# Performance work log

Hardware: AMD Instinct MI355X
Metric: run time of the kernel (lower is better)

The kernel has to match this reference:

```python
import jax, jax.numpy as jnp
import numpy as np

NUM_HEADS = 8
LN_EPS = 1e-5


def _ln(x, g, b):
    mu = x.mean(-1, keepdims=True)
    xc = x - mu
    v = (xc * xc).mean(-1, keepdims=True)
    return xc * jax.lax.rsqrt(v + LN_EPS) * g + b


def setup_inputs() -> dict:
    key = jax.random.key(0)
    B, T, D, NI, NT = 16, 512, 256, 85, 77
    L, FF, TH = 2, 1024, 32
    ks = iter(jax.random.split(key, 40))
    def nrm(shape, std):
        return jax.random.normal(next(ks), shape, jnp.float32) * std
    inp = {
        'img_tokens': nrm((B, NI, D), 1.0),
        'text_tokens': nrm((B, NT, D), 1.0),
        'task_tokens': nrm((T, D), 0.02),
        'type_task': nrm((D,), 0.02),
        'type_img': nrm((D,), 0.02),
        'type_txt': nrm((D,), 0.02),
        'in_ln_g': jnp.ones((D,), jnp.float32), 'in_ln_b': jnp.zeros((D,), jnp.float32),
        'Wqkv': nrm((L, 3 * D, D), 1.0 / np.sqrt(D)), 'bqkv': jnp.zeros((L, 3 * D), jnp.float32),
        'Wo': nrm((L, D, D), 1.0 / np.sqrt(D)), 'bo': jnp.zeros((L, D), jnp.float32),
        'ln1_g': jnp.ones((L, D), jnp.float32), 'ln1_b': jnp.zeros((L, D), jnp.float32),
        'ln2_g': jnp.ones((L, D), jnp.float32), 'ln2_b': jnp.zeros((L, D), jnp.float32),
        'W1': nrm((L, FF, D), 1.0 / np.sqrt(D)), 'b1': jnp.zeros((L, FF), jnp.float32),
        'W2': nrm((L, D, FF), 1.0 / np.sqrt(FF)), 'b2': jnp.zeros((L, D), jnp.float32),
        'out_ln_g': jnp.ones((D,), jnp.float32), 'out_ln_b': jnp.zeros((D,), jnp.float32),
        'tw1': nrm((T, TH, D), 1.0 / np.sqrt(D)), 'tb1': jnp.zeros((T, TH), jnp.float32),
        'tw2': nrm((T, TH), 1.0 / np.sqrt(TH)), 'tb2': jnp.zeros((T,), jnp.float32),
        'text_mask': jnp.arange(NT)[None, :] < jax.random.randint(next(ks), (B, 1), 10, NT + 1),
        'labels': jax.random.randint(next(ks), (B, T), -1, 2),
    }
    return inp


def reference(img_tokens, text_tokens, task_tokens, type_task, type_img, type_txt,
              in_ln_g, in_ln_b, Wqkv, bqkv, Wo, bo, ln1_g, ln1_b, ln2_g, ln2_b,
              W1, b1, W2, b2, out_ln_g, out_ln_b, tw1, tb1, tw2, tb2,
              text_mask, labels):
    B, NI, D = img_tokens.shape
    T = task_tokens.shape[0]
    L = Wqkv.shape[0]
    hd = D // NUM_HEADS
    available = labels != -1                                   # (B, T)
    n_avail = available.sum(axis=1)                            # (B,)
    # Route B: stable-sort available task ids to the front (permutation per row)
    order = jnp.argsort((~available).astype(jnp.int32), axis=1, stable=True)  # (B, T)
    task_toks = task_tokens[order] + type_task                 # (B, T, D)
    seq = jnp.concatenate([task_toks, img_tokens + type_img, text_tokens + type_txt], axis=1)
    seq = _ln(seq, in_ln_g, in_ln_b)
    task_pad = jnp.arange(T)[None, :] >= n_avail[:, None]
    pad = jnp.concatenate([task_pad, jnp.zeros((B, NI), bool), ~text_mask], axis=1)
    bias = jnp.where(pad, -1e9, 0.0).astype(seq.dtype)[:, None, None, :]  # key-padding mask
    scale = 1.0 / np.sqrt(hd)
    S = seq.shape[1]
    for l in range(L):  # pre-LN transformer encoder layers (eval mode)
        h = _ln(seq, ln1_g[l], ln1_b[l])
        qkv = h @ Wqkv[l].T + bqkv[l]
        q, k, v = jnp.split(qkv, 3, axis=-1)
        q = q.reshape(B, S, NUM_HEADS, hd)
        k = k.reshape(B, S, NUM_HEADS, hd)
        v = v.reshape(B, S, NUM_HEADS, hd)
        scores = jnp.einsum('bqhd,bkhd->bhqk', q, k) * scale + bias
        attn = jax.nn.softmax(scores, axis=-1)
        o = jnp.einsum('bhqk,bkhd->bqhd', attn, v).reshape(B, S, D)
        seq = seq + o @ Wo[l].T + bo[l]
        h2 = _ln(seq, ln2_g[l], ln2_b[l])
        seq = seq + jax.nn.gelu(h2 @ W1[l].T + b1[l], approximate=False) @ W2[l].T + b2[l]
    task_out = _ln(seq[:, :T], out_ln_g, out_ln_b)             # (B, T, D)
    # undo the per-row permutation so task t's token sits at column t, then
    # apply all per-task towers as one grouped matmul (MoE dispatch/combine)
    y = jnp.zeros_like(task_out).at[jnp.arange(B)[:, None], order].set(task_out)
    hsz = jax.nn.relu(jnp.einsum('btd,thd->bth', y, tw1) + tb1[None])
    out = jnp.einsum('bth,th->bt', hsz, tw2) + tb2[None]
    return jnp.where(available, out, jnp.zeros((), out.dtype))
```

## Files before the change

kernel.cpp:

```cpp
#include <hip/hip_runtime.h>
#include <hip/hip_bf16.h>
#include <math.h>

constexpr int B_  = 16;
constexpr int T_  = 512;
constexpr int D_  = 256;
constexpr int NI_ = 85;
constexpr int NT_ = 77;
constexpr int S_  = T_ + NI_ + NT_;
constexpr int M_  = B_ * S_;
constexpr int FF_ = 1024;
constexpr int TH_ = 32;
constexpr int NH_ = 8;
constexpr int KT_ = 704;
constexpr int NKT_ = KT_ / 64;

constexpr float MASK_NEG = -30000.0f;

constexpr int N_FT = 26;
constexpr int OFF_[N_FT + 1] = {
    0,
    348160,
    663552,
    794624,
    794880,
    795136,
    795392,
    795648,
    795904,
    1189120,
    1190656,
    1321728,
    1322240,
    1322752,
    1323264,
    1323776,
    1324288,
    1848576,
    1850624,
    2374912,
    2375424,
    2375680,
    2375936,
    6570240,
    6586624,
    6603008,
    6603520
};
constexpr int TOTAL_ELEMS = OFF_[N_FT];

typedef __attribute__((ext_vector_type(8))) short bfrag;
typedef __attribute__((ext_vector_type(4))) float f32x4;

__device__ inline float bf2f(__hip_bfloat16 x) { return __bfloat162float(x); }
__device__ inline __hip_bfloat16 f2bf(float x) { return __float2bfloat16(x); }
__device__ inline float wsum64(float v) {
    #pragma unroll
    for (int m = 32; m >= 1; m >>= 1) v += __shfl_xor(v, m, 64);
    return v;
}
__device__ inline bool is_f32_mode(const void* ln_g_raw) {
    return (*(const unsigned int*)ln_g_raw) == 0x3F800000u;
}

__device__ inline void gload_lds16(const __hip_bfloat16* g, __hip_bfloat16* l) {
#if defined(__has_builtin) && __has_builtin(__builtin_amdgcn_global_load_lds)
    __builtin_amdgcn_global_load_lds(
        (const __attribute__((address_space(1))) unsigned int*)g,
        (__attribute__((address_space(3))) unsigned int*)l, 16, 0, 0);
#else
    *reinterpret_cast<uint4*>(l) = *reinterpret_cast<const uint4*>(g);
#endif
}

struct Ptrs { const void* p[N_FT]; };

__global__ __launch_bounds__(256) void k_convert(Ptrs ptrs, __hip_bfloat16* __restrict__ canon) {
    int idx = blockIdx.x * 256 + threadIdx.x;
    if (idx >= TOTAL_ELEMS) return;
    bool f32 = is_f32_mode(ptrs.p[6]);
    int t = 0;
    #pragma unroll
    for (int i = 1; i < N_FT; i++) if (idx >= OFF_[i]) t = i;
    int local = idx - OFF_[t];
    if (f32) canon[idx] = f2bf(((const float*)ptrs.p[t])[local]);
    else     canon[idx] = ((const __hip_bfloat16*)ptrs.p[t])[local];
}

__global__ void k_prep(const int* __restrict__ labels, int* __restrict__ inv,
                       int* __restrict__ n_avail) {
    __shared__ int sc[T_];
    int b = blockIdx.x, t = threadIdx.x;
    int av = (labels[b * T_ + t] != -1) ? 1 : 0;
    sc[t] = av;
    __syncthreads();
    for (int off = 1; off < T_; off <<= 1) {
        int v = sc[t];
        int u = (t >= off) ? sc[t - off] : 0;
        __syncthreads();
        sc[t] = v + u;
        __syncthreads();
    }
    int incl  = sc[t];
    int excl  = incl - av;
    int total = sc[T_ - 1];
    inv[b * T_ + t] = av ? excl : (total + (t - excl));
    if (t == 0) n_avail[b] = total;
}

__global__ void k_build(const __hip_bfloat16* __restrict__ img,
                        const __hip_bfloat16* __restrict__ txt,
                        const __hip_bfloat16* __restrict__ task,
                        const __hip_bfloat16* __restrict__ ty_task,
                        const __hip_bfloat16* __restrict__ ty_img,
                        const __hip_bfloat16* __restrict__ ty_txt,
                        const __hip_bfloat16* __restrict__ g,
                        const __hip_bfloat16* __restrict__ bln,
                        const __hip_bfloat16* __restrict__ g1,
                        const __hip_bfloat16* __restrict__ b1,
                        const void* __restrict__ text_mask,
                        const int* __restrict__ inv,
                        const int* __restrict__ n_avail,
                        float* __restrict__ seq,
                        __hip_bfloat16* __restrict__ h1,
                        float* __restrict__ bias) {
    int blk = blockIdx.x;
    int b = blk / S_, j = blk % S_;
    int lane = threadIdx.x;

    int dest;
    float bias_v;
    const __hip_bfloat16* src;
    const __hip_bfloat16* tvec;
    if (j < T_) {
        dest = inv[b * T_ + j];
        src = task + (size_t)j * D_;
        tvec = ty_task;
        bias_v = (dest >= n_avail[b]) ? MASK_NEG : 0.f;
    } else if (j < T_ + NI_) {
        dest = j;
        src = img + (size_t)(b * NI_ + (j - T_)) * D_;
        tvec = ty_img;
        bias_v = 0.f;
    } else {
        int x2 = j - T_ - NI_;
        dest = j;
        src = txt + (size_t)(b * NT_ + x2) * D_;
        tvec = ty_txt;
        const unsigned char* mb = (const unsigned char*)text_mask;
        bool is_byte = (mb[1] != 0);
        int mv = is_byte ? (int)mb[b * NT_ + x2]
                         : ((const int*)text_mask)[b * NT_ + x2];
        bias_v = mv ? 0.f : MASK_NEG;
    }

    float x[4];
    float s = 0.f, ss = 0.f;
    #pragma unroll
    for (int i = 0; i < 4; i++) {
        int d = lane * 4 + i;
// ... 32 lines not shown
    *reinterpret_cast<uint2*>(h1 + ((size_t)b * S_ + dest) * D_ + lane * 4) =
        *reinterpret_cast<uint2*>(tmp);
    if (lane == 0) bias[b * S_ + dest] = bias_v;
}

template <int GELU>
__global__ __launch_bounds__(256) void k_gemm(const __hip_bfloat16* __restrict__ A,
                                              const __hip_bfloat16* __restrict__ W,
                                              const __hip_bfloat16* __restrict__ bias,
                                              __hip_bfloat16* __restrict__ Cout,
                                              int Mm, int N, int K) {
    __shared__ __align__(16) unsigned char Sh[24576];
    __hip_bfloat16* As = (__hip_bfloat16*)Sh;
    __hip_bfloat16* Ws = (__hip_bfloat16*)(Sh + 8192);
    __hip_bfloat16* Es = (__hip_bfloat16*)Sh;

    int m0 = blockIdx.x * 64;
    int n0 = blockIdx.y * 128;
    int tid = threadIdx.x;
    int w = tid >> 6, lane = tid & 63;
    int lrow = lane & 15, quad = lane >> 4;

    f32x4 acc[8] = {};

    int kq = (tid & 7) * 8;
    int arow = tid >> 3;
    const __hip_bfloat16* Ar0 = A + (size_t)min(m0 + arow,      Mm - 1) * K + kq;
    const __hip_bfloat16* Ar1 = A + (size_t)min(m0 + arow + 32, Mm - 1) * K + kq;
    __hip_bfloat16* Al0 = As + tid * 8;
    __hip_bfloat16* Al1 = As + (tid + 256) * 8;
    const __hip_bfloat16* Wr[4];
    __hip_bfloat16* Wl[4];
    #pragma unroll
    for (int i = 0; i < 4; i++) {
        int c = tid + i * 256;
        Wr[i] = W + (size_t)(n0 + (c >> 3)) * K + kq;
        Wl[i] = Ws + c * 8;
    }

    for (int k0 = 0; k0 < K; k0 += 64) {
        __syncthreads();
        gload_lds16(Ar0 + k0, Al0);
        gload_lds16(Ar1 + k0, Al1);
        #pragma unroll
        for (int i = 0; i < 4; i++) gload_lds16(Wr[i] + k0, Wl[i]);
        __syncthreads();

        #pragma unroll
        for (int ko = 0; ko < 2; ko++) {
            bfrag af = *reinterpret_cast<const bfrag*>(&As[(w * 16 + lrow) * 64 + ko * 32 + quad * 8]);
            #pragma unroll
            for (int nt = 0; nt < 8; nt++) {
                bfrag bf = *reinterpret_cast<const bfrag*>(&Ws[(nt * 16 + lrow) * 64 + ko * 32 + quad * 8]);
                acc[nt] = __builtin_amdgcn_mfma_f32_16x16x32_bf16(af, bf, acc[nt], 0, 0, 0);
            }
        }
    }
    __syncthreads();

    #pragma unroll
    for (int nt = 0; nt < 8; nt++) {
        int col = nt * 16 + lrow;
        float bv = bf2f(bias[n0 + col]);
        #pragma unroll
        for (int rg = 0; rg < 4; rg++) {
            int row = w * 16 + quad * 4 + rg;
            float v = acc[nt][rg] + bv;
            if (GELU) v = 0.5f * v * (1.f + erff(v * 0.70710678118654752f));
            Es[row * 136 + col] = f2bf(v);
        }
    }
    __syncthreads();

    #pragma unroll
    for (int i = 0; i < 4; i++) {
        int c = tid + i * 256;
        int row = c >> 4, off = (c & 15) * 8;
        int gm = m0 + row;
        if (gm < Mm) {
            uint4 v4 = *reinterpret_cast<const uint4*>(&Es[row * 136 + off]);
            *reinterpret_cast<uint4*>(&Cout[(size_t)gm * N + n0 + off]) = v4;
        }
    }
}

template <int LNOUT>
__global__ __launch_bounds__(256) void k_gemm_lnres(const __hip_bfloat16* __restrict__ A,
                                                    const __hip_bfloat16* __restrict__ W,
                                                    const __hip_bfloat16* __restrict__ bias,
                                                    float* __restrict__ seq,
                                                    const __hip_bfloat16* __restrict__ lng,
                                                    const __hip_bfloat16* __restrict__ lnb,
                                                    __hip_bfloat16* __restrict__ lnout,
                                                    int K) {
    constexpr int N = 256;
    constexpr int ESTRIDE = 260;
    __shared__ __align__(16) unsigned char Sh[36864];
    __hip_bfloat16* As = (__hip_bfloat16*)Sh;
    __hip_bfloat16* Ws = (__hip_bfloat16*)(Sh + 4096);
    float*          Es = (float*)Sh;

    int m0 = blockIdx.x * 32;
    int tid = threadIdx.x;
    int w = tid >> 6, lane = tid & 63;
    int lrow = lane & 15, quad = lane >> 4;

    f32x4 acc[2][4] = {};

    int kq = (tid & 7) * 8;
    const __hip_bfloat16* Ar = A + (size_t)(m0 + (tid >> 3)) * K + kq;
    __hip_bfloat16* Al = As + tid * 8;
    const __hip_bfloat16* Wr[8];
    __hip_bfloat16* Wl[8];
    #pragma unroll
    for (int i = 0; i < 8; i++) {
        int c = tid + i * 256;
        Wr[i] = W + (size_t)(c >> 3) * K + kq;
        Wl[i] = Ws + c * 8;
    }

    for (int k0 = 0; k0 < K; k0 += 64) {
        __syncthreads();
        gload_lds16(Ar + k0, Al);
        #pragma unroll
        for (int i = 0; i < 8; i++) gload_lds16(Wr[i] + k0, Wl[i]);
        __syncthreads();

        #pragma unroll
        for (int ko = 0; ko < 2; ko++) {
            bfrag af[2], bf[4];
            #pragma unroll
            for (int mt = 0; mt < 2; mt++)
                af[mt] = *reinterpret_cast<const bfrag*>(&As[(mt * 16 + lrow) * 64 + ko * 32 + quad * 8]);
            #pragma unroll
            for (int nt = 0; nt < 4; nt++)
                bf[nt] = *reinterpret_cast<const bfrag*>(&Ws[(w * 64 + nt * 16 + lrow) * 64 + ko * 32 + quad * 8]);
            #pragma unroll
            for (int mt = 0; mt < 2; mt++)
                #pragma unroll
                for (int nt = 0; nt < 4; nt++)
                    acc[mt][nt] = __builtin_amdgcn_mfma_f32_16x16x32_bf16(af[mt], bf[nt], acc[mt][nt], 0, 0, 0);
        }
    }
    __syncthreads();

    #pragma unroll
    for (int nt = 0; nt < 4; nt++) {
        int col = w * 64 + nt * 16 + lrow;
        float bv = bf2f(bias[col]);
        #pragma unroll
        for (int mt = 0; mt < 2; mt++)
            #pragma unroll
            for (int rg = 0; rg < 4; rg++)
                Es[(mt * 16 + quad * 4 + rg) * ESTRIDE + col] = acc[mt][nt][rg] + bv;
    }
    __syncthreads();

    int row = tid >> 3, part = tid & 7;
    size_t gm = (size_t)(m0 + row);
    float* seqrow = seq + gm * N + part * 32;
    float t[32];
    float s = 0.f, ss = 0.f;
    #pragma unroll
    for (int j = 0; j < 8; j++) {
        float4 e = *reinterpret_cast<const float4*>(&Es[row * ESTRIDE + part * 32 + j * 4]);
        float4 r4 = *reinterpret_cast<const float4*>(&seqrow[j * 4]);
        float v0 = e.x + r4.x, v1 = e.y + r4.y, v2 = e.z + r4.z, v3 = e.w + r4.w;
        t[j * 4 + 0] = v0; t[j * 4 + 1] = v1; t[j * 4 + 2] = v2; t[j * 4 + 3] = v3;
        s += v0 + v1 + v2 + v3;
        ss += v0 * v0 + v1 * v1 + v2 * v2 + v3 * v3;
    }
    #pragma unroll
    for (int j = 0; j < 8; j++) {
        float4 o = make_float4(t[j * 4 + 0], t[j * 4 + 1], t[j * 4 + 2], t[j * 4 + 3]);
        *reinterpret_cast<float4*>(&seqrow[j * 4]) = o;
    }
    if (LNOUT) {
        #pragma unroll
        for (int mm = 4; mm >= 1; mm >>= 1) {
            s  += __shfl_xor(s,  mm, 8);
            ss += __shfl_xor(ss, mm, 8);
        }
        float mean = s * (1.f / N);
        float var  = ss * (1.f / N) - mean * mean;
        float r    = rsqrtf(fmaxf(var, 0.f) + 1e-5f);
        __hip_bfloat16 ob[32];
        #pragma unroll
        for (int j = 0; j < 32; j++) {
            int col = part * 32 + j;
            ob[j] = f2bf((t[j] - mean) * r * bf2f(lng[col]) + bf2f(lnb[col]));
        }
        #pragma unroll
        for (int j = 0; j < 4; j++)
            *reinterpret_cast<uint4*>(&lnout[gm * N + part * 32 + j * 8]) =
                *reinterpret_cast<const uint4*>(&ob[j * 8]);
    }
}

__global__ __launch_bounds__(256) void k_fattn(const __hip_bfloat16* __restrict__ qkv,
                                               const float* __restrict__ bias,
                                               __hip_bfloat16* __restrict__ out) {
    __shared__ __align__(16) __hip_bfloat16 Vt[2][32 * 72];
    __shared__ __align__(16) __hip_bfloat16 Ps[4][16 * 72];
    __shared__ float Bs[KT_];
    __shared__ int alive[NKT_];
    __shared__ int tlist[NKT_ + 1];
    __shared__ int nact_s;
    int b = blockIdx.z, h = blockIdx.y;
    int tid = threadIdx.x;
    int wave = tid >> 6, lane = tid & 63;
    int lrow = lane & 15, quad = lane >> 4;
    int q0 = blockIdx.x * 64 + wave * 16;

    const float scale = 0.17677669529663687f;
    const __hip_bfloat16* base = qkv + (size_t)b * S_ * 768;
    const float* brow = bias + b * S_;

    for (int i = tid; i < KT_; i += 256) Bs[i] = (i < S_) ? brow[i] : MASK_NEG;
    if (tid < NKT_) alive[tid] = 0;
    __syncthreads();
    for (int i = tid; i < KT_; i += 256)
        if (Bs[i] != MASK_NEG) alive[i >> 6] = 1;
    __syncthreads();
    if (tid == 0) {
        int n = 0;
        for (int t = 0; t < NKT_; t++) if (alive[t]) tlist[n++] = t;
        if (n == 0) { tlist[0] = 0; n = 1; }
        tlist[n] = tlist[n - 1];
        nact_s = n;
    }
    __syncthreads();
    int nact = nact_s;

    int qr = q0 + lrow; if (qr >= S_) qr = S_ - 1;
    bfrag qf = *reinterpret_cast<const bfrag*>(base + (size_t)qr * 768 + h * 32 + quad * 8);

    bfrag ones_f;
    #pragma unroll
    for (int i = 0; i < 8; i++) ((short*)&ones_f)[i] = (short)0x3F80;

    float m[4] = {-3e38f, -3e38f, -3e38f, -3e38f};
    f32x4 Lacc = {};
    f32x4 O[2] = {};

    int skey = lane;
    int sd   = wave * 8;

    bfrag kf_cur[4], vv_cur;
    {
        int k0 = tlist[0] * 64;
        #pragma unroll
        for (int nt = 0; nt < 4; nt++) {
            int kr = min(k0 + nt * 16 + lrow, S_ - 1);
            kf_cur[nt] = *reinterpret_cast<const bfrag*>(base + (size_t)kr * 768 + 256 + h * 32 + quad * 8);
        }
        int kr = min(k0 + skey, S_ - 1);
        vv_cur = *reinterpret_cast<const bfrag*>(base + (size_t)kr * 768 + 512 + h * 32 + sd);
    }

    for (int i = 0; i < nact; i++) {
        int k0 = tlist[i] * 64;
        __hip_bfloat16* vb = Vt[i & 1];

        #pragma unroll
        for (int j = 0; j < 8; j++) vb[(sd + j) * 72 + skey] = ((const __hip_bfloat16*)&vv_cur)[j];
        __syncthreads();

        bfrag kf_nxt[4], vv_nxt;
        {
            int kb = tlist[i + 1] * 64;
            #pragma unroll
            for (int nt = 0; nt < 4; nt++) {
                int kr = min(kb + nt * 16 + lrow, S_ - 1);
                kf_nxt[nt] = *reinterpret_cast<const bfrag*>(base + (size_t)kr * 768 + 256 + h * 32 + quad * 8);
            }
            int kr = min(kb + skey, S_ - 1);
            vv_nxt = *reinterpret_cast<const bfrag*>(base + (size_t)kr * 768 + 512 + h * 32 + sd);
        }

        f32x4 sc4[4];
        #pragma unroll
        for (int nt = 0; nt < 4; nt++) {
            f32x4 z = {};
            sc4[nt] = __builtin_amdgcn_mfma_f32_16x16x32_bf16(qf, kf_cur[nt], z, 0, 0, 0);
            float bv = Bs[k0 + nt * 16 + lrow];
            #pragma unroll
            for (int rg = 0; rg < 4; rg++) sc4[nt][rg] = sc4[nt][rg] * scale + bv;
        }

        float alpha[4];
        #pragma unroll
        for (int rg = 0; rg < 4; rg++) {
            float rm = fmaxf(fmaxf(sc4[0][rg], sc4[1][rg]), fmaxf(sc4[2][rg], sc4[3][rg]));
            #pragma unroll
            for (int mm2 = 1; mm2 <= 8; mm2 <<= 1) rm = fmaxf(rm, __shfl_xor(rm, mm2, 64));
            float mn = fmaxf(m[rg], rm);
            alpha[rg] = __expf(m[rg] - mn);
            m[rg] = mn;
            #pragma unroll
            for (int nt = 0; nt < 4; nt++) sc4[nt][rg] = __expf(sc4[nt][rg] - mn);
        }
        #pragma unroll
        for (int rg = 0; rg < 4; rg++) {
            O[0][rg] *= alpha[rg];
            O[1][rg] *= alpha[rg];
            Lacc[rg] *= alpha[rg];
        }

        #pragma unroll
        for (int nt = 0; nt < 4; nt++)
            #pragma unroll
            for (int rg = 0; rg < 4; rg++)
                Ps[wave][(quad * 4 + rg) * 72 + nt * 16 + lrow] = f2bf(sc4[nt][rg]);

        bfrag ap0 = *reinterpret_cast<const bfrag*>(&Ps[wave][lrow * 72 + quad * 8]);
        bfrag ap1 = *reinterpret_cast<const bfrag*>(&Ps[wave][lrow * 72 + 32 + quad * 8]);
        #pragma unroll
        for (int dt = 0; dt < 2; dt++) {
            bfrag bv0 = *reinterpret_cast<const bfrag*>(&vb[(dt * 16 + lrow) * 72 + quad * 8]);
            bfrag bv1 = *reinterpret_cast<const bfrag*>(&vb[(dt * 16 + lrow) * 72 + 32 + quad * 8]);
            O[dt] = __builtin_amdgcn_mfma_f32_16x16x32_bf16(ap0, bv0, O[dt], 0, 0, 0);
            O[dt] = __builtin_amdgcn_mfma_f32_16x16x32_bf16(ap1, bv1, O[dt], 0, 0, 0);
        }
        Lacc = __builtin_amdgcn_mfma_f32_16x16x32_bf16(ap0, ones_f, Lacc, 0, 0, 0);
        Lacc = __builtin_amdgcn_mfma_f32_16x16x32_bf16(ap1, ones_f, Lacc, 0, 0, 0);

        #pragma unroll
        for (int nt = 0; nt < 4; nt++) kf_cur[nt] = kf_nxt[nt];
        vv_cur = vv_nxt;
    }

    #pragma unroll
    for (int rg = 0; rg < 4; rg++) {
        int qrow = q0 + quad * 4 + rg;
        if (qrow < S_) {
            float invl = 1.f / Lacc[rg];
            #pragma unroll
            for (int dt = 0; dt < 2; dt++)
                out[((size_t)b * S_ + qrow) * D_ + h * 32 + dt * 16 + lrow] = f2bf(O[dt][rg] * invl);
        }
    }
}

__global__ __launch_bounds__(256) void k_final(const float* __restrict__ seq,
                                               const int* __restrict__ inv,
                                               const int* __restrict__ labels,
                                               const __hip_bfloat16* __restrict__ g,
                                               const __hip_bfloat16* __restrict__ bb,
                                               const __hip_bfloat16* __restrict__ tw1,
                                               const __hip_bfloat16* __restrict__ tb1,
                                               const __hip_bfloat16* __restrict__ tw2,
                                               const __hip_bfloat16* __restrict__ tb2,
                                               const void* __restrict__ ln_g_raw,
                                               void* __restrict__ out) {
    int idx = blockIdx.x;
    int t = idx >> 4, b = idx & 15;
    int tid = threadIdx.x;
    bool f32o = is_f32_mode(ln_g_raw);

    int lab = labels[b * T_ + t];
    if (lab == -1) {
        if (tid == 0) {
            if (f32o) ((float*)out)[b * T_ + t] = 0.f;
            else      ((__hip_bfloat16*)out)[b * T_ + t] = f2bf(0.f);
        }
        return;
    }

    __shared__ float y[D_];
    __shared__ float hb[TH_];
    __shared__ float rs[4], rq[4];

    int row = inv[b * T_ + t];
    float x = seq[((size_t)b * S_ + row) * D_ + tid];
    float s1 = wsum64(x);
    float s2 = wsum64(x * x);
    int w = tid >> 6, lane = tid & 63;
    if (lane == 0) { rs[w] = s1; rq[w] = s2; }
    __syncthreads();
    float fs = rs[0] + rs[1] + rs[2] + rs[3];
    float fq = rq[0] + rq[1] + rq[2] + rq[3];
    float mean = fs * (1.f / D_);
    float var  = fq * (1.f / D_) - mean * mean;
    float r    = rsqrtf(fmaxf(var, 0.f) + 1e-5f);
    y[tid] = (x - mean) * r * bf2f(g[tid]) + bf2f(bb[tid]);
    __syncthreads();

    int hh = tid >> 3, part = tid & 7;
    const uint4* w4 = reinterpret_cast<const uint4*>(tw1 + ((size_t)t * TH_ + hh) * D_ + part * 32);
    float acc = 0.f;
    #pragma unroll
    for (int i = 0; i < 4; i++) {
        uint4 kv = w4[i];
        unsigned int wd[4] = {kv.x, kv.y, kv.z, kv.w};
        #pragma unroll
        for (int j2 = 0; j2 < 4; j2++) {
            unsigned int lo = wd[j2] << 16, hi = wd[j2] & 0xffff0000u;
            float flo, fhi;
            __builtin_memcpy(&flo, &lo, 4);
            __builtin_memcpy(&fhi, &hi, 4);
            acc += y[part * 32 + i * 8 + j2 * 2] * flo;
            acc += y[part * 32 + i * 8 + j2 * 2 + 1] * fhi;
        }
    }
    #pragma unroll
    for (int mm = 4; mm >= 1; mm >>= 1) acc += __shfl_down(acc, mm, 8);
    if (part == 0) {
        float hz = acc + bf2f(tb1[t * TH_ + hh]);
        hz = fmaxf(hz, 0.f);
        hb[hh] = hz * bf2f(tw2[t * TH_ + hh]);
    }
    __syncthreads();
    if (tid == 0) {
        float o = bf2f(tb2[t]);
        #pragma unroll
        for (int i = 0; i < TH_; i++) o += hb[i];
        if (f32o) ((float*)out)[b * T_ + t] = o;
        else      ((__hip_bfloat16*)out)[b * T_ + t] = f2bf(o);
    }
}

extern "C" void kernel_launch(void* const* d_in, const int* in_sizes, int n_in,
                              void* d_out, int out_size, void* d_ws, size_t ws_size,
                              hipStream_t stream) {
    const void* tmask  = d_in[26];
    const int*  labels = (const int*)d_in[27];

    char* p = (char*)d_ws;
    auto alloc = [&](size_t bytes) {
        char* r = p;
        p += (bytes + 255) & ~size_t(255);
        return r;
    };
    __hip_bfloat16* canon  = (__hip_bfloat16*)alloc(sizeof(__hip_bfloat16) * (size_t)TOTAL_ELEMS);
    int*            inv     = (int*)alloc(sizeof(int) * B_ * T_);
    int*            n_avail = (int*)alloc(sizeof(int) * B_);
    float*          bias    = (float*)alloc(sizeof(float) * M_);
    float*          seqF    = (float*)alloc(sizeof(float) * (size_t)M_ * D_);
    __hip_bfloat16* bufA    = (__hip_bfloat16*)alloc(sizeof(__hip_bfloat16) * (size_t)M_ * D_);
    __hip_bfloat16* bufBig  = (__hip_bfloat16*)alloc(sizeof(__hip_bfloat16) * (size_t)M_ * FF_);

    Ptrs ptrs;
    for (int i = 0; i < N_FT; i++) ptrs.p[i] = d_in[i];
    hipLaunchKernelGGL(k_convert, dim3((TOTAL_ELEMS + 255) / 256), dim3(256), 0, stream,
                       ptrs, canon);

    const __hip_bfloat16* img      = canon + OFF_[0];
    const __hip_bfloat16* txt      = canon + OFF_[1];
    const __hip_bfloat16* task     = canon + OFF_[2];
    const __hip_bfloat16* ty_task  = canon + OFF_[3];
    const __hip_bfloat16* ty_img   = canon + OFF_[4];
    const __hip_bfloat16* ty_txt   = canon + OFF_[5];
    const __hip_bfloat16* in_ln_g  = canon + OFF_[6];
    const __hip_bfloat16* in_ln_b  = canon + OFF_[7];
    const __hip_bfloat16* Wqkv     = canon + OFF_[8];
    const __hip_bfloat16* bqkv     = canon + OFF_[9];
    const __hip_bfloat16* Wo       = canon + OFF_[10];
    const __hip_bfloat16* bo       = canon + OFF_[11];
    const __hip_bfloat16* ln1_g    = canon + OFF_[12];
    const __hip_bfloat16* ln1_b    = canon + OFF_[13];
    const __hip_bfloat16* ln2_g    = canon + OFF_[14];
    const __hip_bfloat16* ln2_b    = canon + OFF_[15];
    const __hip_bfloat16* W1       = canon + OFF_[16];
    const __hip_bfloat16* b1       = canon + OFF_[17];
    const __hip_bfloat16* W2       = canon + OFF_[18];
    const __hip_bfloat16* b2       = canon + OFF_[19];
    const __hip_bfloat16* out_ln_g = canon + OFF_[20];
    const __hip_bfloat16* out_ln_b = canon + OFF_[21];
    const __hip_bfloat16* tw1      = canon + OFF_[22];
    const __hip_bfloat16* tb1      = canon + OFF_[23];
    const __hip_bfloat16* tw2      = canon + OFF_[24];
    const __hip_bfloat16* tb2      = canon + OFF_[25];

    hipLaunchKernelGGL(k_prep, dim3(B_), dim3(T_), 0, stream, labels, inv, n_avail);
    hipLaunchKernelGGL(k_build, dim3(B_ * S_), dim3(64), 0, stream,
                       img, txt, task, ty_task, ty_img, ty_txt, in_ln_g, in_ln_b,
                       ln1_g, ln1_b, tmask, inv, n_avail, seqF, bufA, bias);

    const int mtiles = (M_ + 63) / 64;
    const int rtiles = M_ / 32;
    const int qtiles = (S_ + 63) / 64;

    for (int l = 0; l < 2; l++) {
        hipLaunchKernelGGL((k_gemm<0>), dim3(mtiles, 6), dim3(256), 0, stream,
                           bufA, Wqkv + (size_t)l * 3 * D_ * D_, bqkv + l * 3 * D_,
                           bufBig, M_, 3 * D_, D_);
        hipLaunchKernelGGL(k_fattn, dim3(qtiles, NH_, B_), dim3(256), 0, stream,
                           bufBig, bias, bufA);
        hipLaunchKernelGGL((k_gemm_lnres<1>), dim3(rtiles), dim3(256), 0, stream,
                           bufA, Wo + (size_t)l * D_ * D_, bo + l * D_, seqF,
                           ln2_g + l * D_, ln2_b + l * D_, bufA, D_);
        hipLaunchKernelGGL((k_gemm<1>), dim3(mtiles, 8), dim3(256), 0, stream,
                           bufA, W1 + (size_t)l * FF_ * D_, b1 + l * FF_,
                           bufBig, M_, FF_, D_);
        if (l == 0) {
            hipLaunchKernelGGL((k_gemm_lnres<1>), dim3(rtiles), dim3(256), 0, stream,
                               bufBig, W2 + (size_t)l * D_ * FF_, b2 + l * D_, seqF,
                               ln1_g + 1 * D_, ln1_b + 1 * D_, bufA, FF_);
        } else {
            hipLaunchKernelGGL((k_gemm_lnres<0>), dim3(rtiles), dim3(256), 0, stream,
                               bufBig, W2 + (size_t)l * D_ * FF_, b2 + l * D_, seqF,
                               (const __hip_bfloat16*)nullptr, (const __hip_bfloat16*)nullptr,
                               (__hip_bfloat16*)nullptr, FF_);
        }
    }

    hipLaunchKernelGGL(k_final, dim3(T_ * B_), dim3(256), 0, stream,
                       seqF, inv, labels, out_ln_g, out_ln_b,
                       tw1, tb1, tw2, tb2, d_in[6], d_out);
}
```

Before: 403.4 us.

## Fuse out-projection, LN2, FFN up/GELU/down and residual into one tail kernel

Replaces the Wo GEMM+LN kernel, the W1 GELU GEMM and the W2 GEMM+residual kernel with a single per-32-row kernel. The attention tile, the LN2 output and the FFN hidden activations (in two 512-column halves) stay in shared memory. This removes the large M×1024 hidden-activation round trip through global memory and two launches. In exchange, weight fragments are read directly from global memory without LDS staging, and each 32-row block rereads the full Wo/W1/W2, so it relies on cache hits. Larger LDS use may also lower occupancy.

```diff
diff --git a/kernel.cpp b/kernel.cpp
--- a/kernel.cpp
+++ b/kernel.cpp
@@ -54,6 +54,9 @@
 
 __device__ inline float bf2f(__hip_bfloat16 x) { return __bfloat162float(x); }
 __device__ inline __hip_bfloat16 f2bf(float x) { return __float2bfloat16(x); }
+__device__ inline f32x4 mfma16(bfrag a, bfrag b, f32x4 c) {
+    return __builtin_amdgcn_mfma_f32_16x16x32_bf16(a, b, c, 0, 0, 0);
+}
 __device__ inline float wsum64(float v) {
     #pragma unroll
     for (int m = 32; m >= 1; m >>= 1) v += __shfl_xor(v, m, 64);
@@ -244,7 +247,7 @@
             #pragma unroll
             for (int nt = 0; nt < 8; nt++) {
                 bfrag bf = *reinterpret_cast<const bfrag*>(&Ws[(nt * 16 + lrow) * 64 + ko * 32 + quad * 8]);
-                acc[nt] = __builtin_amdgcn_mfma_f32_16x16x32_bf16(af, bf, acc[nt], 0, 0, 0);
+                acc[nt] = mfma16(af, bf, acc[nt]);
             }
         }
     }
@@ -277,115 +280,197 @@
 }
 
 template <int LNOUT>
-__global__ __launch_bounds__(256) void k_gemm_lnres(const __hip_bfloat16* __restrict__ A,
-                                                    const __hip_bfloat16* __restrict__ W,
-                                                    const __hip_bfloat16* __restrict__ bias,
-                                                    float* __restrict__ seq,
-                                                    const __hip_bfloat16* __restrict__ lng,
-                                                    const __hip_bfloat16* __restrict__ lnb,
-                                                    __hip_bfloat16* __restrict__ lnout,
-                                                    int K) {
-    constexpr int N = 256;
-    constexpr int ESTRIDE = 260;
-    __shared__ __align__(16) unsigned char Sh[36864];
-    __hip_bfloat16* As = (__hip_bfloat16*)Sh;
-    __hip_bfloat16* Ws = (__hip_bfloat16*)(Sh + 4096);
-    float*          Es = (float*)Sh;
+__global__ __launch_bounds__(256) void k_tail(const __hip_bfloat16* __restrict__ attn,
+                                              const __hip_bfloat16* __restrict__ Wo,
+                                              const __hip_bfloat16* __restrict__ bo,
+                                              float* __restrict__ seq,
+                                              const __hip_bfloat16* __restrict__ ln2g,
+                                              const __hip_bfloat16* __restrict__ ln2b,
+                                              const __hip_bfloat16* __restrict__ W1,
+                                              const __hip_bfloat16* __restrict__ b1,
+                                              const __hip_bfloat16* __restrict__ W2,
+                                              const __hip_bfloat16* __restrict__ b2,
+                                              const __hip_bfloat16* __restrict__ lng,
+                                              const __hip_bfloat16* __restrict__ lnb,
+                                              __hip_bfloat16* __restrict__ hout) {
+    constexpr int ASTR = 264;
+    constexpr int FSTR = 520;
+    constexpr int ESTR = 260;
+    __shared__ __align__(16) unsigned char Sh[16896 + 33280];
+    __hip_bfloat16* Atile = (__hip_bfloat16*)Sh;
+    __hip_bfloat16* h2    = (__hip_bfloat16*)Sh;
+    __hip_bfloat16* fh    = (__hip_bfloat16*)(Sh + 16896);
+    float*          Es    = (float*)(Sh + 16896);
 
     int m0 = blockIdx.x * 32;
     int tid = threadIdx.x;
-    int w = tid >> 6, lane = tid & 63;
+    int wave = tid >> 6, lane = tid & 63;
     int lrow = lane & 15, quad = lane >> 4;
 
-    f32x4 acc[2][4] = {};
-
-    int kq = (tid & 7) * 8;
-    const __hip_bfloat16* Ar = A + (size_t)(m0 + (tid >> 3)) * K + kq;
-    __hip_bfloat16* Al = As + tid * 8;
-    const __hip_bfloat16* Wr[8];
-    __hip_bfloat16* Wl[8];
-    #pragma unroll
-    for (int i = 0; i < 8; i++) {
+    #pragma unroll
+    for (int i = 0; i < 4; i++) {
         int c = tid + i * 256;
-        Wr[i] = W + (size_t)(c >> 3) * K + kq;
-        Wl[i] = Ws + c * 8;
-    }
-
-    for (int k0 = 0; k0 < K; k0 += 64) {
-        __syncthreads();
-        gload_lds16(Ar + k0, Al);
-        #pragma unroll
-        for (int i = 0; i < 8; i++) gload_lds16(Wr[i] + k0, Wl[i]);
-        __syncthreads();
-
-        #pragma unroll
-        for (int ko = 0; ko < 2; ko++) {
-            bfrag af[2], bf[4];
-            #pragma unroll
-            for (int mt = 0; mt < 2; mt++)
-                af[mt] = *reinterpret_cast<const bfrag*>(&As[(mt * 16 + lrow) * 64 + ko * 32 + quad * 8]);
-            #pragma unroll
-            for (int nt = 0; nt < 4; nt++)
-                bf[nt] = *reinterpret_cast<const bfrag*>(&Ws[(w * 64 + nt * 16 + lrow) * 64 + ko * 32 + quad * 8]);
+        int row = c >> 5;
+        int off = (c & 31) * 8;
+        uint4 v = *reinterpret_cast<const uint4*>(attn + (size_t)(m0 + row) * 256 + off);
+        *reinterpret_cast<uint4*>(&Atile[row * ASTR + off]) = v;
+    }
+    __syncthreads();
+
+    int wn = wave * 64;
+    {
+        f32x4 a1[2][4] = {};
+        for (int k = 0; k < 8; k++) {
+            bfrag af0 = *reinterpret_cast<const bfrag*>(&Atile[lrow * ASTR + k * 32 + quad * 8]);
+            bfrag af1 = *reinterpret_cast<const bfrag*>(&Atile[(16 + lrow) * ASTR + k * 32 + quad * 8]);
+            #pragma unroll
+            for (int nt = 0; nt < 4; nt++) {
+                bfrag bf = *reinterpret_cast<const bfrag*>(Wo + (size_t)(wn + nt * 16 + lrow) * 256 + k * 32 + quad * 8);
+                a1[0][nt] = mfma16(af0, bf, a1[0][nt]);
+                a1[1][nt] = mfma16(af1, bf, a1[1][nt]);
+            }
+        }
+        #pragma unroll
+        for (int nt = 0; nt < 4; nt++) {
+            int col = wn + nt * 16 + lrow;
+            float bv = bf2f(bo[col]);
             #pragma unroll
             for (int mt = 0; mt < 2; mt++)
                 #pragma unroll
-                for (int nt = 0; nt < 4; nt++)
-                    acc[mt][nt] = __builtin_amdgcn_mfma_f32_16x16x32_bf16(af[mt], bf[nt], acc[mt][nt], 0, 0, 0);
-        }
-    }
-    __syncthreads();
-
-    #pragma unroll
-    for (int nt = 0; nt < 4; nt++) {
-        int col = w * 64 + nt * 16 + lrow;
-        float bv = bf2f(bias[col]);
-        #pragma unroll
-        for (int mt = 0; mt < 2; mt++)
-            #pragma unroll
-            for (int rg = 0; rg < 4; rg++)
-                Es[(mt * 16 + quad * 4 + rg) * ESTRIDE + col] = acc[mt][nt][rg] + bv;
-    }
-    __syncthreads();
-
-    int row = tid >> 3, part = tid & 7;
-    size_t gm = (size_t)(m0 + row);
-    float* seqrow = seq + gm * N + part * 32;
-    float t[32];
-    float s = 0.f, ss = 0.f;
-    #pragma unroll
-    for (int j = 0; j < 8; j++) {
-        float4 e = *reinterpret_cast<const float4*>(&Es[row * ESTRIDE + part * 32 + j * 4]);
-        float4 r4 = *reinterpret_cast<const float4*>(&seqrow[j * 4]);
-        float v0 = e.x + r4.x, v1 = e.y + r4.y, v2 = e.z + r4.z, v3 = e.w + r4.w;
-        t[j * 4 + 0] = v0; t[j * 4 + 1] = v1; t[j * 4 + 2] = v2; t[j * 4 + 3] = v3;
-        s += v0 + v1 + v2 + v3;
-        ss += v0 * v0 + v1 * v1 + v2 * v2 + v3 * v3;
-    }
-    #pragma unroll
-    for (int j = 0; j < 8; j++) {
-        float4 o = make_float4(t[j * 4 + 0], t[j * 4 + 1], t[j * 4 + 2], t[j * 4 + 3]);
-        *reinterpret_cast<float4*>(&seqrow[j * 4]) = o;
-    }
-    if (LNOUT) {
+                for (int rg = 0; rg < 4; rg++)
+                    Es[(mt * 16 + quad * 4 + rg) * ESTR + col] = a1[mt][nt][rg] + bv;
+        }
+    }
+    __syncthreads();
+
+    {
+        int row = tid >> 3, part = tid & 7;
+        size_t gm = (size_t)(m0 + row);
+        float* srow = seq + gm * 256 + part * 32;
+        float t[32];
+        float s = 0.f, ss = 0.f;
+        #pragma unroll
+        for (int j = 0; j < 8; j++) {
+            float4 e = *reinterpret_cast<const float4*>(&Es[row * ESTR + part * 32 + j * 4]);
+            float4 r = *reinterpret_cast<const float4*>(&srow[j * 4]);
+            float v0 = e.x + r.x, v1 = e.y + r.y, v2 = e.z + r.z, v3 = e.w + r.w;
+            t[j * 4] = v0; t[j * 4 + 1] = v1; t[j * 4 + 2] = v2; t[j * 4 + 3] = v3;
+            s += v0 + v1 + v2 + v3;
+            ss += v0 * v0 + v1 * v1 + v2 * v2 + v3 * v3;
+            *reinterpret_cast<float4*>(&srow[j * 4]) = make_float4(v0, v1, v2, v3);
+        }
         #pragma unroll
         for (int mm = 4; mm >= 1; mm >>= 1) {
             s  += __shfl_xor(s,  mm, 8);
             ss += __shfl_xor(ss, mm, 8);
         }
-        float mean = s * (1.f / N);
-        float var  = ss * (1.f / N) - mean * mean;
-        float r    = rsqrtf(fmaxf(var, 0.f) + 1e-5f);
+        float mean = s * (1.f / 256.f);
+        float var  = ss * (1.f / 256.f) - mean * mean;
+        float rr   = rsqrtf(fmaxf(var, 0.f) + 1e-5f);
         __hip_bfloat16 ob[32];
         #pragma unroll
         for (int j = 0; j < 32; j++) {
             int col = part * 32 + j;
-            ob[j] = f2bf((t[j] - mean) * r * bf2f(lng[col]) + bf2f(lnb[col]));
+            ob[j] = f2bf((t[j] - mean) * rr * bf2f(ln2g[col]) + bf2f(ln2b[col]));
         }
         #pragma unroll
         for (int j = 0; j < 4; j++)
-            *reinterpret_cast<uint4*>(&lnout[gm * N + part * 32 + j * 8]) =
+            *reinterpret_cast<uint4*>(&h2[row * ASTR + part * 32 + j * 8]) =
                 *reinterpret_cast<const uint4*>(&ob[j * 8]);
+    }
+    __syncthreads();
+
+    int wn1 = wave * 128;
+    f32x4 a4[2][4] = {};
+    for (int half = 0; half < 2; half++) {
+        f32x4 a3[2][8] = {};
+        for (int k = 0; k < 8; k++) {
+            bfrag af0 = *reinterpret_cast<const bfrag*>(&h2[lrow * ASTR + k * 32 + quad * 8]);
+            bfrag af1 = *reinterpret_cast<const bfrag*>(&h2[(16 + lrow) * ASTR + k * 32 + quad * 8]);
+            #pragma unroll
+            for (int nt = 0; nt < 8; nt++) {
+                int n = half * 512 + wn1 + nt * 16 + lrow;
+                bfrag bf = *reinterpret_cast<const bfrag*>(W1 + (size_t)n * 256 + k * 32 + quad * 8);
+                a3[0][nt] = mfma16(af0, bf, a3[0][nt]);
+                a3[1][nt] = mfma16(af1, bf, a3[1][nt]);
+            }
+        }
+        __syncthreads();
+        #pragma unroll
+        for (int nt = 0; nt < 8; nt++) {
+            int lcol = wn1 + nt * 16 + lrow;
+            float bv = bf2f(b1[half * 512 + lcol]);
+            #pragma unroll
+            for (int mt = 0; mt < 2; mt++)
+                #pragma unroll
+                for (int rg = 0; rg < 4; rg++) {
+                    float v = a3[mt][nt][rg] + bv;
+                    v = 0.5f * v * (1.f + erff(v * 0.70710678118654752f));
+                    fh[(mt * 16 + quad * 4 + rg) * FSTR + lcol] = f2bf(v);
+                }
+        }
+        __syncthreads();
+        for (int k = 0; k < 16; k++) {
+            bfrag af0 = *reinterpret_cast<const bfrag*>(&fh[lrow * FSTR + k * 32 + quad * 8]);
+            bfrag af1 = *reinterpret_cast<const bfrag*>(&fh[(16 + lrow) * FSTR + k * 32 + quad * 8]);
+            #pragma unroll
+            for (int nt = 0; nt < 4; nt++) {
+                bfrag bf = *reinterpret_cast<const bfrag*>(W2 + (size_t)(wn + nt * 16 + lrow) * 1024 + half * 512 + k * 32 + quad * 8);
+                a4[0][nt] = mfma16(af0, bf, a4[0][nt]);
+                a4[1][nt] = mfma16(af1, bf, a4[1][nt]);
+            }
+        }
+    }
+    __syncthreads();
+
+    #pragma unroll
+    for (int nt = 0; nt < 4; nt++) {
+        int col = wn + nt * 16 + lrow;
+        float bv = bf2f(b2[col]);
+        #pragma unroll
+        for (int mt = 0; mt < 2; mt++)
+            #pragma unroll
+            for (int rg = 0; rg < 4; rg++)
+                Es[(mt * 16 + quad * 4 + rg) * ESTR + col] = a4[mt][nt][rg] + bv;
+    }
+    __syncthreads();
+
+    {
+        int row = tid >> 3, part = tid & 7;
+        size_t gm = (size_t)(m0 + row);
+        float* srow = seq + gm * 256 + part * 32;
+        float t[32];
+        float s = 0.f, ss = 0.f;
+        #pragma unroll
+        for (int j = 0; j < 8; j++) {
+            float4 e = *reinterpret_cast<const float4*>(&Es[row * ESTR + part * 32 + j * 4]);
+            float4 r = *reinterpret_cast<const float4*>(&srow[j * 4]);
+            float v0 = e.x + r.x, v1 = e.y + r.y, v2 = e.z + r.z, v3 = e.w + r.w;
+            t[j * 4] = v0; t[j * 4 + 1] = v1; t[j * 4 + 2] = v2; t[j * 4 + 3] = v3;
+            s += v0 + v1 + v2 + v3;
+            ss += v0 * v0 + v1 * v1 + v2 * v2 + v3 * v3;
+            *reinterpret_cast<float4*>(&srow[j * 4]) = make_float4(v0, v1, v2, v3);
+        }
+        if (LNOUT) {
+            #pragma unroll
+            for (int mm = 4; mm >= 1; mm >>= 1) {
+                s  += __shfl_xor(s,  mm, 8);
+                ss += __shfl_xor(ss, mm, 8);
+            }
+            float mean = s * (1.f / 256.f);
+            float var  = ss * (1.f / 256.f) - mean * mean;
+            float rr   = rsqrtf(fmaxf(var, 0.f) + 1e-5f);
+            __hip_bfloat16 ob[32];
+            #pragma unroll
+            for (int j = 0; j < 32; j++) {
+                int col = part * 32 + j;
+                ob[j] = f2bf((t[j] - mean) * rr * bf2f(lng[col]) + bf2f(lnb[col]));
+            }
+            #pragma unroll
+            for (int j = 0; j < 4; j++)
+                *reinterpret_cast<uint4*>(&hout[gm * 256 + part * 32 + j * 8]) =
+                    *reinterpret_cast<const uint4*>(&ob[j * 8]);
+        }
     }
 }
 
@@ -474,7 +559,7 @@
         #pragma unroll
         for (int nt = 0; nt < 4; nt++) {
             f32x4 z = {};
-            sc4[nt] = __builtin_amdgcn_mfma_f32_16x16x32_bf16(qf, kf_cur[nt], z, 0, 0, 0);
+            sc4[nt] = mfma16(qf, kf_cur[nt], z);
             float bv = Bs[k0 + nt * 16 + lrow];
             #pragma unroll
             for (int rg = 0; rg < 4; rg++) sc4[nt][rg] = sc4[nt][rg] * scale + bv;
@@ -511,11 +596,11 @@
         for (int dt = 0; dt < 2; dt++) {
             bfrag bv0 = *reinterpret_cast<const bfrag*>(&vb[(dt * 16 + lrow) * 72 + quad * 8]);
             bfrag bv1 = *reinterpret_cast<const bfrag*>(&vb[(dt * 16 + lrow) * 72 + 32 + quad * 8]);
-            O[dt] = __builtin_amdgcn_mfma_f32_16x16x32_bf16(ap0, bv0, O[dt], 0, 0, 0);
-            O[dt] = __builtin_amdgcn_mfma_f32_16x16x32_bf16(ap1, bv1, O[dt], 0, 0, 0);
-        }
-        Lacc = __builtin_amdgcn_mfma_f32_16x16x32_bf16(ap0, ones_f, Lacc, 0, 0, 0);
-        Lacc = __builtin_amdgcn_mfma_f32_16x16x32_bf16(ap1, ones_f, Lacc, 0, 0, 0);
+            O[dt] = mfma16(ap0, bv0, O[dt]);
+            O[dt] = mfma16(ap1, bv1, O[dt]);
+        }
+        Lacc = mfma16(ap0, ones_f, Lacc);
+        Lacc = mfma16(ap1, ones_f, Lacc);
 
         #pragma unroll
         for (int nt = 0; nt < 4; nt++) kf_cur[nt] = kf_nxt[nt];
@@ -630,7 +715,7 @@
     float*          bias    = (float*)alloc(sizeof(float) * M_);
     float*          seqF    = (float*)alloc(sizeof(float) * (size_t)M_ * D_);
     __hip_bfloat16* bufA    = (__hip_bfloat16*)alloc(sizeof(__hip_bfloat16) * (size_t)M_ * D_);
-    __hip_bfloat16* bufBig  = (__hip_bfloat16*)alloc(sizeof(__hip_bfloat16) * (size_t)M_ * FF_);
+    __hip_bfloat16* bufBig  = (__hip_bfloat16*)alloc(sizeof(__hip_bfloat16) * (size_t)M_ * 3 * D_);
 
     Ptrs ptrs;
     for (int i = 0; i < N_FT; i++) ptrs.p[i] = d_in[i];
@@ -679,21 +764,21 @@
                            bufBig, M_, 3 * D_, D_);
         hipLaunchKernelGGL(k_fattn, dim3(qtiles, NH_, B_), dim3(256), 0, stream,
                            bufBig, bias, bufA);
-        hipLaunchKernelGGL((k_gemm_lnres<1>), dim3(rtiles), dim3(256), 0, stream,
-                           bufA, Wo + (size_t)l * D_ * D_, bo + l * D_, seqF,
-                           ln2_g + l * D_, ln2_b + l * D_, bufA, D_);
-        hipLaunchKernelGGL((k_gemm<1>), dim3(mtiles, 8), dim3(256), 0, stream,
-                           bufA, W1 + (size_t)l * FF_ * D_, b1 + l * FF_,
-                           bufBig, M_, FF_, D_);
         if (l == 0) {
-            hipLaunchKernelGGL((k_gemm_lnres<1>), dim3(rtiles), dim3(256), 0, stream,
-                               bufBig, W2 + (size_t)l * D_ * FF_, b2 + l * D_, seqF,
-                               ln1_g + 1 * D_, ln1_b + 1 * D_, bufA, FF_);
+            hipLaunchKernelGGL((k_tail<1>), dim3(rtiles), dim3(256), 0, stream,
+                               bufA, Wo + (size_t)l * D_ * D_, bo + l * D_, seqF,
+                               ln2_g + l * D_, ln2_b + l * D_,
+                               W1 + (size_t)l * FF_ * D_, b1 + l * FF_,
+                               W2 + (size_t)l * D_ * FF_, b2 + l * D_,
+                               ln1_g + 1 * D_, ln1_b + 1 * D_, bufA);
         } else {
-            hipLaunchKernelGGL((k_gemm_lnres<0>), dim3(rtiles), dim3(256), 0, stream,
-                               bufBig, W2 + (size_t)l * D_ * FF_, b2 + l * D_, seqF,
+            hipLaunchKernelGGL((k_tail<0>), dim3(rtiles), dim3(256), 0, stream,
+                               bufA, Wo + (size_t)l * D_ * D_, bo + l * D_, seqF,
+                               ln2_g + l * D_, ln2_b + l * D_,
+                               W1 + (size_t)l * FF_ * D_, b1 + l * FF_,
+                               W2 + (size_t)l * D_ * FF_, b2 + l * D_,
                                (const __hip_bfloat16*)nullptr, (const __hip_bfloat16*)nullptr,
-                               (__hip_bfloat16*)nullptr, FF_);
+                               (__hip_bfloat16*)nullptr);
         }
     }
 
```

Measured after the change: 505.6 us. 25.3% more time.

## Double query rows per attention wave and merge convert/prep kernels

Applied to the files above, without the earlier changes.

Each attention wave now handles 32 query rows (two 16-row MFMA tiles) instead of 16, so every K/V tile it loads and stages is reused across twice as many queries. The query tile per block grows to 128 and the grid shrinks by half. The bias load and alive-tile detection are folded into one loop. The input conversion and label prefix-scan kernels are merged into one launch to remove a launch. The trade-off is more registers and LDS per wave and fewer blocks, which may lower occupancy.

```diff
diff --git a/kernel.cpp b/kernel.cpp
--- a/kernel.cpp
+++ b/kernel.cpp
@@ -48,6 +48,7 @@
     6603520
 };
 constexpr int TOTAL_ELEMS = OFF_[N_FT];
+constexpr int CONV_BLOCKS = (TOTAL_ELEMS + 511) / 512;
 
 typedef __attribute__((ext_vector_type(8))) short bfrag;
 typedef __attribute__((ext_vector_type(4))) float f32x4;
@@ -75,37 +76,39 @@
 
 struct Ptrs { const void* p[N_FT]; };
 
-__global__ __launch_bounds__(256) void k_convert(Ptrs ptrs, __hip_bfloat16* __restrict__ canon) {
-    int idx = blockIdx.x * 256 + threadIdx.x;
-    if (idx >= TOTAL_ELEMS) return;
-    bool f32 = is_f32_mode(ptrs.p[6]);
-    int t = 0;
-    #pragma unroll
-    for (int i = 1; i < N_FT; i++) if (idx >= OFF_[i]) t = i;
-    int local = idx - OFF_[t];
-    if (f32) canon[idx] = f2bf(((const float*)ptrs.p[t])[local]);
-    else     canon[idx] = ((const __hip_bfloat16*)ptrs.p[t])[local];
-}
-
-__global__ void k_prep(const int* __restrict__ labels, int* __restrict__ inv,
-                       int* __restrict__ n_avail) {
-    __shared__ int sc[T_];
-    int b = blockIdx.x, t = threadIdx.x;
-    int av = (labels[b * T_ + t] != -1) ? 1 : 0;
-    sc[t] = av;
-    __syncthreads();
-    for (int off = 1; off < T_; off <<= 1) {
-        int v = sc[t];
-        int u = (t >= off) ? sc[t - off] : 0;
+__global__ __launch_bounds__(512) void k_init(Ptrs ptrs, __hip_bfloat16* __restrict__ canon,
+                                              const int* __restrict__ labels,
+                                              int* __restrict__ inv,
+                                              int* __restrict__ n_avail) {
+    if (blockIdx.x < CONV_BLOCKS) {
+        int idx = blockIdx.x * 512 + threadIdx.x;
+        if (idx >= TOTAL_ELEMS) return;
+        bool f32 = is_f32_mode(ptrs.p[6]);
+        int t = 0;
+        #pragma unroll
+        for (int i = 1; i < N_FT; i++) if (idx >= OFF_[i]) t = i;
+        int local = idx - OFF_[t];
+        if (f32) canon[idx] = f2bf(((const float*)ptrs.p[t])[local]);
+        else     canon[idx] = ((const __hip_bfloat16*)ptrs.p[t])[local];
+    } else {
+        __shared__ int sc[T_];
+        int b = blockIdx.x - CONV_BLOCKS, t = threadIdx.x;
+        int av = (labels[b * T_ + t] != -1) ? 1 : 0;
+        sc[t] = av;
         __syncthreads();
-        sc[t] = v + u;
-        __syncthreads();
-    }
-    int incl  = sc[t];
-    int excl  = incl - av;
-    int total = sc[T_ - 1];
-    inv[b * T_ + t] = av ? excl : (total + (t - excl));
-    if (t == 0) n_avail[b] = total;
+        for (int off = 1; off < T_; off <<= 1) {
+            int v = sc[t];
+            int u = (t >= off) ? sc[t - off] : 0;
+            __syncthreads();
+            sc[t] = v + u;
+            __syncthreads();
+        }
+        int incl  = sc[t];
+        int excl  = incl - av;
+        int total = sc[T_ - 1];
+        inv[b * T_ + t] = av ? excl : (total + (t - excl));
+        if (t == 0) n_avail[b] = total;
+    }
 }
 
 __global__ void k_build(const __hip_bfloat16* __restrict__ img,
@@ -393,7 +396,7 @@
                                                const float* __restrict__ bias,
                                                __hip_bfloat16* __restrict__ out) {
     __shared__ __align__(16) __hip_bfloat16 Vt[2][32 * 72];
-    __shared__ __align__(16) __hip_bfloat16 Ps[4][16 * 72];
+    __shared__ __align__(16) __hip_bfloat16 Ps[4][32 * 72];
     __shared__ float Bs[KT_];
     __shared__ int alive[NKT_];
     __shared__ int tlist[NKT_ + 1];
@@ -402,17 +405,19 @@
     int tid = threadIdx.x;
     int wave = tid >> 6, lane = tid & 63;
     int lrow = lane & 15, quad = lane >> 4;
-    int q0 = blockIdx.x * 64 + wave * 16;
+    int q0 = blockIdx.x * 128 + wave * 32;
 
     const float scale = 0.17677669529663687f;
     const __hip_bfloat16* base = qkv + (size_t)b * S_ * 768;
     const float* brow = bias + b * S_;
 
-    for (int i = tid; i < KT_; i += 256) Bs[i] = (i < S_) ? brow[i] : MASK_NEG;
     if (tid < NKT_) alive[tid] = 0;
     __syncthreads();
-    for (int i = tid; i < KT_; i += 256)
-        if (Bs[i] != MASK_NEG) alive[i >> 6] = 1;
+    for (int i = tid; i < KT_; i += 256) {
+        float v = (i < S_) ? brow[i] : MASK_NEG;
+        Bs[i] = v;
+        if (v != MASK_NEG) alive[i >> 6] = 1;
+    }
     __syncthreads();
     if (tid == 0) {
         int n = 0;
@@ -424,16 +429,25 @@
     __syncthreads();
     int nact = nact_s;
 
-    int qr = q0 + lrow; if (qr >= S_) qr = S_ - 1;
-    bfrag qf = *reinterpret_cast<const bfrag*>(base + (size_t)qr * 768 + h * 32 + quad * 8);
+    bfrag qf[2];
+    {
+        int qr0 = min(q0 + lrow, S_ - 1);
+        int qr1 = min(q0 + 16 + lrow, S_ - 1);
+        qf[0] = *reinterpret_cast<const bfrag*>(base + (size_t)qr0 * 768 + h * 32 + quad * 8);
+        qf[1] = *reinterpret_cast<const bfrag*>(base + (size_t)qr1 * 768 + h * 32 + quad * 8);
+    }
 
     bfrag ones_f;
     #pragma unroll
     for (int i = 0; i < 8; i++) ((short*)&ones_f)[i] = (short)0x3F80;
 
-    float m[4] = {-3e38f, -3e38f, -3e38f, -3e38f};
-    f32x4 Lacc = {};
-    f32x4 O[2] = {};
+    float m[2][4];
+    #pragma unroll
+    for (int qh = 0; qh < 2; qh++)
+        #pragma unroll
+        for (int rg = 0; rg < 4; rg++) m[qh][rg] = -3e38f;
+    f32x4 Lacc[2] = {};
+    f32x4 O[2][2] = {};
 
     int skey = lane;
     int sd   = wave * 8;
@@ -470,52 +484,60 @@
             vv_nxt = *reinterpret_cast<const bfrag*>(base + (size_t)kr * 768 + 512 + h * 32 + sd);
         }
 
-        f32x4 sc4[4];
+        f32x4 sc[2][4];
         #pragma unroll
         for (int nt = 0; nt < 4; nt++) {
-            f32x4 z = {};
-            sc4[nt] = __builtin_amdgcn_mfma_f32_16x16x32_bf16(qf, kf_cur[nt], z, 0, 0, 0);
             float bv = Bs[k0 + nt * 16 + lrow];
             #pragma unroll
-            for (int rg = 0; rg < 4; rg++) sc4[nt][rg] = sc4[nt][rg] * scale + bv;
-        }
-
-        float alpha[4];
-        #pragma unroll
-        for (int rg = 0; rg < 4; rg++) {
-            float rm = fmaxf(fmaxf(sc4[0][rg], sc4[1][rg]), fmaxf(sc4[2][rg], sc4[3][rg]));
-            #pragma unroll
-            for (int mm2 = 1; mm2 <= 8; mm2 <<= 1) rm = fmaxf(rm, __shfl_xor(rm, mm2, 64));
-            float mn = fmaxf(m[rg], rm);
-            alpha[rg] = __expf(m[rg] - mn);
-            m[rg] = mn;
-            #pragma unroll
-            for (int nt = 0; nt < 4; nt++) sc4[nt][rg] = __expf(sc4[nt][rg] - mn);
-        }
-        #pragma unroll
-        for (int rg = 0; rg < 4; rg++) {
-            O[0][rg] *= alpha[rg];
-            O[1][rg] *= alpha[rg];
-            Lacc[rg] *= alpha[rg];
-        }
-
-        #pragma unroll
-        for (int nt = 0; nt < 4; nt++)
-            #pragma unroll
-            for (int rg = 0; rg < 4; rg++)
-                Ps[wave][(quad * 4 + rg) * 72 + nt * 16 + lrow] = f2bf(sc4[nt][rg]);
-
-        bfrag ap0 = *reinterpret_cast<const bfrag*>(&Ps[wave][lrow * 72 + quad * 8]);
-        bfrag ap1 = *reinterpret_cast<const bfrag*>(&Ps[wave][lrow * 72 + 32 + quad * 8]);
-        #pragma unroll
-        for (int dt = 0; dt < 2; dt++) {
-            bfrag bv0 = *reinterpret_cast<const bfrag*>(&vb[(dt * 16 + lrow) * 72 + quad * 8]);
-            bfrag bv1 = *reinterpret_cast<const bfrag*>(&vb[(dt * 16 + lrow) * 72 + 32 + quad * 8]);
-            O[dt] = __builtin_amdgcn_mfma_f32_16x16x32_bf16(ap0, bv0, O[dt], 0, 0, 0);
-            O[dt] = __builtin_amdgcn_mfma_f32_16x16x32_bf16(ap1, bv1, O[dt], 0, 0, 0);
-        }
-        Lacc = __builtin_amdgcn_mfma_f32_16x16x32_bf16(ap0, ones_f, Lacc, 0, 0, 0);
-        Lacc = __builtin_amdgcn_mfma_f32_16x16x32_bf16(ap1, ones_f, Lacc, 0, 0, 0);
+            for (int qh = 0; qh < 2; qh++) {
+                f32x4 z = {};
+                sc[qh][nt] = __builtin_amdgcn_mfma_f32_16x16x32_bf16(qf[qh], kf_cur[nt], z, 0, 0, 0);
+                #pragma unroll
+                for (int rg = 0; rg < 4; rg++) sc[qh][nt][rg] = sc[qh][nt][rg] * scale + bv;
+            }
+        }
+
+        #pragma unroll
+        for (int qh = 0; qh < 2; qh++) {
+            float alpha[4];
+            #pragma unroll
+            for (int rg = 0; rg < 4; rg++) {
+                float rm = fmaxf(fmaxf(sc[qh][0][rg], sc[qh][1][rg]), fmaxf(sc[qh][2][rg], sc[qh][3][rg]));
+                #pragma unroll
+                for (int mm2 = 1; mm2 <= 8; mm2 <<= 1) rm = fmaxf(rm, __shfl_xor(rm, mm2, 64));
+                float mn = fmaxf(m[qh][rg], rm);
+                alpha[rg] = __expf(m[qh][rg] - mn);
+                m[qh][rg] = mn;
+                #pragma unroll
+                for (int nt = 0; nt < 4; nt++) sc[qh][nt][rg] = __expf(sc[qh][nt][rg] - mn);
+            }
+            #pragma unroll
+            for (int rg = 0; rg < 4; rg++) {
+                O[qh][0][rg] *= alpha[rg];
+                O[qh][1][rg] *= alpha[rg];
+                Lacc[qh][rg] *= alpha[rg];
+            }
+            #pragma unroll
+            for (int nt = 0; nt < 4; nt++)
+                #pragma unroll
+                for (int rg = 0; rg < 4; rg++)
+                    Ps[wave][(qh * 16 + quad * 4 + rg) * 72 + nt * 16 + lrow] = f2bf(sc[qh][nt][rg]);
+        }
+
+        #pragma unroll
+        for (int qh = 0; qh < 2; qh++) {
+            bfrag ap0 = *reinterpret_cast<const bfrag*>(&Ps[wave][(qh * 16 + lrow) * 72 + quad * 8]);
+            bfrag ap1 = *reinterpret_cast<const bfrag*>(&Ps[wave][(qh * 16 + lrow) * 72 + 32 + quad * 8]);
+            #pragma unroll
+            for (int dt = 0; dt < 2; dt++) {
+                bfrag bv0 = *reinterpret_cast<const bfrag*>(&vb[(dt * 16 + lrow) * 72 + quad * 8]);
+                bfrag bv1 = *reinterpret_cast<const bfrag*>(&vb[(dt * 16 + lrow) * 72 + 32 + quad * 8]);
+                O[qh][dt] = __builtin_amdgcn_mfma_f32_16x16x32_bf16(ap0, bv0, O[qh][dt], 0, 0, 0);
+                O[qh][dt] = __builtin_amdgcn_mfma_f32_16x16x32_bf16(ap1, bv1, O[qh][dt], 0, 0, 0);
+            }
+            Lacc[qh] = __builtin_amdgcn_mfma_f32_16x16x32_bf16(ap0, ones_f, Lacc[qh], 0, 0, 0);
+            Lacc[qh] = __builtin_amdgcn_mfma_f32_16x16x32_bf16(ap1, ones_f, Lacc[qh], 0, 0, 0);
+        }
 
         #pragma unroll
         for (int nt = 0; nt < 4; nt++) kf_cur[nt] = kf_nxt[nt];
@@ -523,15 +545,17 @@
     }
 
     #pragma unroll
-    for (int rg = 0; rg < 4; rg++) {
-        int qrow = q0 + quad * 4 + rg;
-        if (qrow < S_) {
-            float invl = 1.f / Lacc[rg];
-            #pragma unroll
-            for (int dt = 0; dt < 2; dt++)
-                out[((size_t)b * S_ + qrow) * D_ + h * 32 + dt * 16 + lrow] = f2bf(O[dt][rg] * invl);
-        }
-    }
+    for (int qh = 0; qh < 2; qh++)
+        #pragma unroll
+        for (int rg = 0; rg < 4; rg++) {
+            int qrow = q0 + qh * 16 + quad * 4 + rg;
+            if (qrow < S_) {
+                float invl = 1.f / Lacc[qh][rg];
+                #pragma unroll
+                for (int dt = 0; dt < 2; dt++)
+                    out[((size_t)b * S_ + qrow) * D_ + h * 32 + dt * 16 + lrow] = f2bf(O[qh][dt][rg] * invl);
+            }
+        }
 }
 
 __global__ __launch_bounds__(256) void k_final(const float* __restrict__ seq,
@@ -634,8 +658,8 @@
 
     Ptrs ptrs;
     for (int i = 0; i < N_FT; i++) ptrs.p[i] = d_in[i];
-    hipLaunchKernelGGL(k_convert, dim3((TOTAL_ELEMS + 255) / 256), dim3(256), 0, stream,
-                       ptrs, canon);
+    hipLaunchKernelGGL(k_init, dim3(CONV_BLOCKS + B_), dim3(512), 0, stream,
+                       ptrs, canon, labels, inv, n_avail);
 
     const __hip_bfloat16* img      = canon + OFF_[0];
     const __hip_bfloat16* txt      = canon + OFF_[1];
@@ -664,14 +688,13 @@
     const __hip_bfloat16* tw2      = canon + OFF_[24];
     const __hip_bfloat16* tb2      = canon + OFF_[25];
 
-    hipLaunchKernelGGL(k_prep, dim3(B_), dim3(T_), 0, stream, labels, inv, n_avail);
     hipLaunchKernelGGL(k_build, dim3(B_ * S_), dim3(64), 0, stream,
                        img, txt, task, ty_task, ty_img, ty_txt, in_ln_g, in_ln_b,
                        ln1_g, ln1_b, tmask, inv, n_avail, seqF, bufA, bias);
 
     const int mtiles = (M_ + 63) / 64;
     const int rtiles = M_ / 32;
-    const int qtiles = (S_ + 63) / 64;
+    const int qtiles = (S_ + 127) / 128;
 
     for (int l = 0; l < 2; l++) {
         hipLaunchKernelGGL((k_gemm<0>), dim3(mtiles, 6), dim3(256), 0, stream,
```

Result: faster. 393.6 us (-2.4%).
